# Optimization experiments

Measured on AMD Instinct MI355X. Metric: run time of the kernel, lower is better.

Reference implementation:

```python
import jax, jax.numpy as jnp
import numpy as np

IN, E, BSZ, A, J, NC, BATCH = 784, 512, 8, 2, 7, 128, 512
T = BSZ ** A  # 64 blocks


def setup_inputs() -> dict:
    key = jax.random.key(0)
    ks = jax.random.split(key, 10)
    s = lambda k, sh: (jax.random.normal(k, sh, jnp.float32) * 0.02)
    return {
        "x": jax.random.normal(ks[0], (BATCH, IN), jnp.float32),
        "emb_W": s(ks[1], (IN, E)), "emb_b": jnp.zeros((E,), jnp.float32),
        # stacked per-block state_transform: Linear(E,E)-ReLU-Linear(E,E)-ReLU
        "st_W1": s(ks[2], (T, E, E)), "st_b1": jnp.zeros((T, E), jnp.float32),
        "st_W2": s(ks[3], (T, E, E)), "st_b2": jnp.zeros((T, E), jnp.float32),
        # stacked per-block address_transform: Linear(E,E)-ReLU-Linear(E,A*BSZ)
        "ad_W1": s(ks[4], (T, E, E)), "ad_b1": jnp.zeros((T, E), jnp.float32),
        "ad_W2": s(ks[5], (T, E, A * BSZ)), "ad_b2": jnp.zeros((T, A * BSZ), jnp.float32),
        # output head: Linear(E,E)-ReLU-Linear(E,NC)
        "out_W1": s(ks[6], (E, E)), "out_b1": jnp.zeros((E,), jnp.float32),
        "out_W2": s(ks[7], (E, NC)), "out_b2": jnp.zeros((NC,), jnp.float32),
    }


def reference(x, emb_W, emb_b, st_W1, st_b1, st_W2, st_b2,
              ad_W1, ad_b1, ad_W2, ad_b2, out_W1, out_b1, out_W2, out_b2):
    strides = BSZ ** jnp.arange(A - 1, -1, -1)  # row-major flat index

    def flat_idx(addr):  # [B, A] -> [B]
        return jnp.sum(addr * strides, axis=1)

    def next_address(state, idx):
        # block's address_transform; argmax(softmax(logits)) == argmax(logits)
        h = jax.nn.relu(jnp.einsum("be,beh->bh", state, ad_W1[idx]) + ad_b1[idx])
        logits = jnp.einsum("bh,bho->bo", h, ad_W2[idx]) + ad_b2[idx]
        return jnp.argmax(logits.reshape(-1, A, BSZ), axis=2)  # [B, A]

    def through_block(state, idx):
        h = jax.nn.relu(jnp.einsum("be,beh->bh", state, st_W1[idx]) + st_b1[idx])
        t = jax.nn.relu(jnp.einsum("bh,bho->bo", h, st_W2[idx]) + st_b2[idx])
        norm = jnp.linalg.norm(state, axis=1, keepdims=True)
        return t / (norm + 1e-6)

    state = x.reshape(x.shape[0], -1) @ emb_W + emb_b  # [B, E]
    initial_state = state
    B = state.shape[0]
    # initial address from brain_blocks[0]
    addr = next_address(initial_state, jnp.zeros((B,), jnp.int32))

    for i in range(J):  # small fixed jump count
        idx = flat_idx(addr)
        t = through_block(state, idx)           # normalized transformed state
        addr = next_address(t, idx)             # address from transformed state
        state = t + (i / max(1, J - 1)) * initial_state  # residual ramp

    final = through_block(state, flat_idx(addr)) + initial_state
    h = jax.nn.relu(final @ out_W1 + out_b1)
    return h @ out_W2 + out_b2  # [B, NC]
```

## Files before the change

kernel.cpp:

```cpp
#include <hip/hip_runtime.h>

namespace {

constexpr int B     = 512;
constexpr int IN_F  = 784;
constexpr int E     = 512;
constexpr int ABSZ  = 16;
constexpr int J     = 7;
constexpr int NC    = 128;
constexpr int NT    = 256;

__device__ inline void matvec512(const float* __restrict__ W,
                                 const float* __restrict__ bias,
                                 const float* __restrict__ vin,
                                 float* __restrict__ vout,
                                 int tid, bool do_relu)
{
    const int o = 2 * tid;
    float a0 = 0.f, a1 = 0.f;
    const float* wp = W + o;
    #pragma unroll 8
    for (int e = 0; e < E; ++e) {
        const float v = vin[e];
        const float2 w = *reinterpret_cast<const float2*>(wp + (size_t)e * E);
        a0 = fmaf(v, w.x, a0);
        a1 = fmaf(v, w.y, a1);
    }
    a0 += bias[o];
    a1 += bias[o + 1];
    if (do_relu) { a0 = fmaxf(a0, 0.f); a1 = fmaxf(a1, 0.f); }
    vout[o]     = a0;
    vout[o + 1] = a1;
}

__device__ inline int next_address(const float* __restrict__ ad_W1,
                                   const float* __restrict__ ad_b1,
                                   const float* __restrict__ ad_W2,
                                   const float* __restrict__ ad_b2,
                                   int idx,
                                   const float* __restrict__ vin,
                                   float* __restrict__ s_h,
                                   float* __restrict__ s_part,
                                   float* __restrict__ s_logits,
                                   int* __restrict__ s_idx_p,
                                   int tid)
{
    matvec512(ad_W1 + (size_t)idx * E * E, ad_b1 + (size_t)idx * E, vin, s_h, tid, true);
    __syncthreads();

    {
        const int o  = tid & (ABSZ - 1);
        const int e0 = tid >> 4;
        const float* w2 = ad_W2 + (size_t)idx * E * ABSZ;
        float acc = 0.f;
        #pragma unroll 4
        for (int e = e0; e < E; e += 16) {
            acc = fmaf(s_h[e], w2[(size_t)e * ABSZ + o], acc);
        }
        s_part[tid] = acc;
    }
    __syncthreads();
    if (tid < ABSZ) {
        float sum = ad_b2[(size_t)idx * ABSZ + tid];
        #pragma unroll
        for (int k = 0; k < 16; ++k) sum += s_part[tid + 16 * k];
        s_logits[tid] = sum;
    }
    __syncthreads();
    if (tid == 0) {
        int a0 = 0, a1 = 0;
        float m0 = s_logits[0], m1 = s_logits[8];
        #pragma unroll
        for (int k = 1; k < 8; ++k) {
            if (s_logits[k]     > m0) { m0 = s_logits[k];     a0 = k; }
            if (s_logits[8 + k] > m1) { m1 = s_logits[8 + k]; a1 = k; }
        }
        *s_idx_p = a0 * 8 + a1;
    }
    __syncthreads();
    return *s_idx_p;
}

__device__ inline void through_block(const float* __restrict__ st_W1,
                                     const float* __restrict__ st_b1,
                                     const float* __restrict__ st_W2,
                                     const float* __restrict__ st_b2,
                                     int idx,
                                     const float* __restrict__ s_state,
                                     float* __restrict__ s_h,
                                     float* __restrict__ s_t,
                                     float* __restrict__ s_part,
                                     float* __restrict__ s_scale,
                                     int tid)
{
    matvec512(st_W1 + (size_t)idx * E * E, st_b1 + (size_t)idx * E, s_state, s_h, tid, true);

    {
        const int o = 2 * tid;
        float v0 = s_state[o], v1 = s_state[o + 1];
        float ss = v0 * v0 + v1 * v1;
        #pragma unroll
        for (int off = 32; off > 0; off >>= 1) ss += __shfl_down(ss, off, 64);
        if ((tid & 63) == 0) s_part[tid >> 6] = ss;
    }
    __syncthreads();
    if (tid == 0) {
        float tot = s_part[0] + s_part[1] + s_part[2] + s_part[3];
        *s_scale = 1.0f / (sqrtf(tot) + 1e-6f);
    }
    matvec512(st_W2 + (size_t)idx * E * E, st_b2 + (size_t)idx * E, s_h, s_t, tid, true);
    __syncthreads();
    {
        const float sc = *s_scale;
        const int o = 2 * tid;
        s_t[o]     *= sc;
        s_t[o + 1] *= sc;
    }
    __syncthreads();
}

__global__ __launch_bounds__(NT) void brain_kernel(
    const float* __restrict__ x,
    const float* __restrict__ emb_W,  const float* __restrict__ emb_b,
    const float* __restrict__ st_W1,  const float* __restrict__ st_b1,
    const float* __restrict__ st_W2,  const float* __restrict__ st_b2,
    const float* __restrict__ ad_W1,  const float* __restrict__ ad_b1,
    const float* __restrict__ ad_W2,  const float* __restrict__ ad_b2,
    const float* __restrict__ out_W1, const float* __restrict__ out_b1,
    const float* __restrict__ out_W2, const float* __restrict__ out_b2,
    float* __restrict__ out)
{
    const int b   = blockIdx.x;
    const int tid = threadIdx.x;

    __shared__ float s_x[IN_F];
    __shared__ float s_state[E];
    __shared__ float s_init[E];
    __shared__ float s_h[E];
    __shared__ float s_t[E];
    __shared__ float s_part[NT];
    __shared__ float s_logits[ABSZ];
    __shared__ float s_scale;
    __shared__ int   s_idx;

    for (int i = tid; i < IN_F; i += NT) s_x[i] = x[(size_t)b * IN_F + i];
    __syncthreads();

    {
        const int o = 2 * tid;
        float a0 = 0.f, a1 = 0.f;
        const float* wp = emb_W + o;
        #pragma unroll 4
        for (int i = 0; i < IN_F; ++i) {
            const float v = s_x[i];
            const float2 w = *reinterpret_cast<const float2*>(wp + (size_t)i * E);
            a0 = fmaf(v, w.x, a0);
            a1 = fmaf(v, w.y, a1);
        }
        a0 += emb_b[o];
        a1 += emb_b[o + 1];
        s_state[o]     = a0;  s_state[o + 1] = a1;
        s_init[o]      = a0;  s_init[o + 1]  = a1;
    }
    __syncthreads();

    int idx = next_address(ad_W1, ad_b1, ad_W2, ad_b2, 0, s_init,
                           s_h, s_part, s_logits, &s_idx, tid);

    for (int i = 0; i < J; ++i) {
        through_block(st_W1, st_b1, st_W2, st_b2, idx,
                      s_state, s_h, s_t, s_part, &s_scale, tid);
        const int nidx = next_address(ad_W1, ad_b1, ad_W2, ad_b2, idx, s_t,
                                      s_h, s_part, s_logits, &s_idx, tid);
        {
            const float ramp = (float)i * (1.0f / 6.0f);
            const int o = 2 * tid;
            s_state[o]     = s_t[o]     + ramp * s_init[o];
            s_state[o + 1] = s_t[o + 1] + ramp * s_init[o + 1];
        }
        __syncthreads();
        idx = nidx;
    }

    through_block(st_W1, st_b1, st_W2, st_b2, idx,
                  s_state, s_h, s_t, s_part, &s_scale, tid);
    {
        const int o = 2 * tid;
        s_state[o]     = s_t[o]     + s_init[o];
        s_state[o + 1] = s_t[o + 1] + s_init[o + 1];
    }
    __syncthreads();

    matvec512(out_W1, out_b1, s_state, s_h, tid, true);
    __syncthreads();

    {
        const int oo = tid & (NC - 1);
        const int e0 = tid >> 7;
        float acc = 0.f;
        #pragma unroll 4
        for (int e = e0; e < E; e += 2) {
            acc = fmaf(s_h[e], out_W2[(size_t)e * NC + oo], acc);
        }
        s_part[tid] = acc;
    }
    __syncthreads();
    if (tid < NC) {
        out[(size_t)b * NC + tid] = out_b2[tid] + s_part[tid] + s_part[tid + NC];
    }
}

}

extern "C" void kernel_launch(void* const* d_in, const int* in_sizes, int n_in,
                              void* d_out, int out_size, void* d_ws, size_t ws_size,
                              hipStream_t stream)
{
    const float* x      = (const float*)d_in[0];
    const float* emb_W  = (const float*)d_in[1];
    const float* emb_b  = (const float*)d_in[2];
    const float* st_W1  = (const float*)d_in[3];
    const float* st_b1  = (const float*)d_in[4];
    const float* st_W2  = (const float*)d_in[5];
    const float* st_b2  = (const float*)d_in[6];
    const float* ad_W1  = (const float*)d_in[7];
    const float* ad_b1  = (const float*)d_in[8];
    const float* ad_W2  = (const float*)d_in[9];
    const float* ad_b2  = (const float*)d_in[10];
    const float* out_W1 = (const float*)d_in[11];
    const float* out_b1 = (const float*)d_in[12];
    const float* out_W2 = (const float*)d_in[13];
    const float* out_b2 = (const float*)d_in[14];
    float* out = (float*)d_out;

    hipLaunchKernelGGL(brain_kernel, dim3(B), dim3(NT), 0, stream,
                       x, emb_W, emb_b, st_W1, st_b1, st_W2, st_b2,
                       ad_W1, ad_b1, ad_W2, ad_b2,
                       out_W1, out_b1, out_W2, out_b2, out);
}
```

Measured before the change: 1.755 ms.

## Replace per-sample fused kernel with bucketed multi-kernel batched matvec pipeline

The single per-sample kernel, which streamed a full 512x512 weight matrix per sample per layer, is replaced by a sequence of kernels. Each jump now groups samples by their block index (bucket kernel), so every weight tile is loaded once and applied to up to eight rows of the same block. Norm, residual ramp and argmax are folded into small per-row kernels. This cuts weight traffic roughly by the bucket occupancy, at the cost of about 40 kernel launches, a single-block bucketing step with a serial prefix scan, and intermediates round-tripping through global memory.

```diff
diff --git a/kernel.cpp b/kernel.cpp
--- a/kernel.cpp
+++ b/kernel.cpp
@@ -2,72 +2,197 @@
 
 namespace {
 
-constexpr int B     = 512;
-constexpr int IN_F  = 784;
-constexpr int E     = 512;
-constexpr int ABSZ  = 16;
-constexpr int J     = 7;
-constexpr int NC    = 128;
-constexpr int NT    = 256;
-
-__device__ inline void matvec512(const float* __restrict__ W,
-                                 const float* __restrict__ bias,
-                                 const float* __restrict__ vin,
-                                 float* __restrict__ vout,
-                                 int tid, bool do_relu)
-{
-    const int o = 2 * tid;
-    float a0 = 0.f, a1 = 0.f;
-    const float* wp = W + o;
-    #pragma unroll 8
-    for (int e = 0; e < E; ++e) {
-        const float v = vin[e];
-        const float2 w = *reinterpret_cast<const float2*>(wp + (size_t)e * E);
-        a0 = fmaf(v, w.x, a0);
-        a1 = fmaf(v, w.y, a1);
-    }
-    a0 += bias[o];
-    a1 += bias[o + 1];
-    if (do_relu) { a0 = fmaxf(a0, 0.f); a1 = fmaxf(a1, 0.f); }
-    vout[o]     = a0;
-    vout[o + 1] = a1;
-}
-
-__device__ inline int next_address(const float* __restrict__ ad_W1,
-                                   const float* __restrict__ ad_b1,
-                                   const float* __restrict__ ad_W2,
-                                   const float* __restrict__ ad_b2,
-                                   int idx,
-                                   const float* __restrict__ vin,
-                                   float* __restrict__ s_h,
-                                   float* __restrict__ s_part,
-                                   float* __restrict__ s_logits,
-                                   int* __restrict__ s_idx_p,
-                                   int tid)
-{
-    matvec512(ad_W1 + (size_t)idx * E * E, ad_b1 + (size_t)idx * E, vin, s_h, tid, true);
+constexpr int B      = 512;
+constexpr int IN_F   = 784;
+constexpr int E      = 512;
+constexpr int T      = 64;
+constexpr int ABSZ   = 16;
+constexpr int J      = 7;
+constexpr int NC     = 128;
+constexpr int TILE_R = 8;
+constexpr int MAXTIL = 128;
+
+__global__ void k_iddesc(int* __restrict__ rows_id, int4* __restrict__ desc_id)
+{
+    const int t = threadIdx.x;
+    rows_id[t] = t;
+    if (t < MAXTIL)
+        desc_id[t] = (t < B / TILE_R) ? make_int4(0, t * TILE_R, TILE_R, 0)
+                                      : make_int4(0, 0, 0, 0);
+}
+
+__global__ __launch_bounds__(256) void k_embed(
+    const float* __restrict__ x, const float* __restrict__ Wm,
+    const float* __restrict__ bias,
+    float* __restrict__ state, float* __restrict__ initv)
+{
+    const int c  = blockIdx.y * 256 + threadIdx.x;
+    const int r0 = blockIdx.x * 8;
+    float acc[8] = {0,0,0,0,0,0,0,0};
+    const float* Wb = Wm + c;
+    for (int e = 0; e < IN_F; e += 4) {
+        const float w0 = Wb[(size_t)(e + 0) * E];
+        const float w1 = Wb[(size_t)(e + 1) * E];
+        const float w2 = Wb[(size_t)(e + 2) * E];
+        const float w3 = Wb[(size_t)(e + 3) * E];
+        #pragma unroll
+        for (int g = 0; g < 8; ++g) {
+            const float4 xv = *reinterpret_cast<const float4*>(
+                x + (size_t)(r0 + g) * IN_F + e);
+            acc[g] = fmaf(xv.x, w0, acc[g]);
+            acc[g] = fmaf(xv.y, w1, acc[g]);
+            acc[g] = fmaf(xv.z, w2, acc[g]);
+            acc[g] = fmaf(xv.w, w3, acc[g]);
+        }
+    }
+    const float bv = bias[c];
+    #pragma unroll
+    for (int g = 0; g < 8; ++g) {
+        const float v = acc[g] + bv;
+        state[(size_t)(r0 + g) * E + c] = v;
+        initv[(size_t)(r0 + g) * E + c] = v;
+    }
+}
+
+__global__ __launch_bounds__(64) void k_norm(const float* __restrict__ state,
+                                             float* __restrict__ norms)
+{
+    const int row = blockIdx.x;
+    const int t   = threadIdx.x;
+    const float4 a = *reinterpret_cast<const float4*>(state + (size_t)row * E + t * 8);
+    const float4 b = *reinterpret_cast<const float4*>(state + (size_t)row * E + t * 8 + 4);
+    float ss = a.x*a.x + a.y*a.y + a.z*a.z + a.w*a.w
+             + b.x*b.x + b.y*b.y + b.z*b.z + b.w*b.w;
+    #pragma unroll
+    for (int off = 32; off > 0; off >>= 1) ss += __shfl_down(ss, off, 64);
+    if (t == 0) norms[row] = sqrtf(ss);
+}
+
+__global__ __launch_bounds__(512) void k_bucket(const int* __restrict__ idx,
+                                                int* __restrict__ rows_sorted,
+                                                int4* __restrict__ desc)
+{
+    __shared__ int cnt[T], off[T], c2[T];
+    const int t = threadIdx.x;
+    if (t < T) { cnt[t] = 0; c2[t] = 0; }
     __syncthreads();
-
-    {
-        const int o  = tid & (ABSZ - 1);
-        const int e0 = tid >> 4;
-        const float* w2 = ad_W2 + (size_t)idx * E * ABSZ;
-        float acc = 0.f;
-        #pragma unroll 4
-        for (int e = e0; e < E; e += 16) {
-            acc = fmaf(s_h[e], w2[(size_t)e * ABSZ + o], acc);
-        }
-        s_part[tid] = acc;
-    }
+    const int my = idx[t];
+    atomicAdd(&cnt[my], 1);
     __syncthreads();
-    if (tid < ABSZ) {
-        float sum = ad_b2[(size_t)idx * ABSZ + tid];
-        #pragma unroll
-        for (int k = 0; k < 16; ++k) sum += s_part[tid + 16 * k];
-        s_logits[tid] = sum;
+    if (t == 0) {
+        int s = 0;
+        for (int b = 0; b < T; ++b) { off[b] = s; s += cnt[b]; }
     }
     __syncthreads();
-    if (tid == 0) {
+    const int p = off[my] + atomicAdd(&c2[my], 1);
+    rows_sorted[p] = t;
+    if (t == 0) {
+        int slot = 0;
+        for (int b = 0; b < T; ++b) {
+            const int G = cnt[b], o = off[b];
+            for (int k = 0; k < G; k += TILE_R)
+                desc[slot++] = make_int4(b, o + k, min(TILE_R, G - k), 0);
+        }
+        for (; slot < MAXTIL; ++slot) desc[slot] = make_int4(0, 0, 0, 0);
+    }
+}
+
+template <bool RELU, bool SCALE, bool ADDINIT>
+__global__ __launch_bounds__(256) void k_mv(
+    const float* __restrict__ in, float* __restrict__ out,
+    const float* __restrict__ W, const float* __restrict__ bias,
+    const int4* __restrict__ desc, const int* __restrict__ rows,
+    const float* __restrict__ norms, const float* __restrict__ initv)
+{
+    const int4 d = desc[blockIdx.x];
+    const int n = d.z;
+    if (n == 0) return;
+    const int blk = d.x, start = d.y;
+    const int c = blockIdx.y * 256 + threadIdx.x;
+    const float* Wb = W + (size_t)blk * E * E + c;
+
+    int rowid[TILE_R];
+    int rbase[TILE_R];
+    #pragma unroll
+    for (int g = 0; g < TILE_R; ++g) {
+        rowid[g] = rows[start + min(g, n - 1)];
+        rbase[g] = rowid[g] * E;
+    }
+
+    float acc[TILE_R] = {0,0,0,0,0,0,0,0};
+    for (int e = 0; e < E; e += 4) {
+        const float w0 = Wb[(size_t)(e + 0) * E];
+        const float w1 = Wb[(size_t)(e + 1) * E];
+        const float w2 = Wb[(size_t)(e + 2) * E];
+        const float w3 = Wb[(size_t)(e + 3) * E];
+        #pragma unroll
+        for (int g = 0; g < TILE_R; ++g) {
+            const float4 sv = *reinterpret_cast<const float4*>(in + rbase[g] + e);
+            acc[g] = fmaf(sv.x, w0, acc[g]);
+            acc[g] = fmaf(sv.y, w1, acc[g]);
+            acc[g] = fmaf(sv.z, w2, acc[g]);
+            acc[g] = fmaf(sv.w, w3, acc[g]);
+        }
+    }
+
+    const float bv = bias[blk * E + c];
+    #pragma unroll
+    for (int g = 0; g < TILE_R; ++g) {
+        if (g < n) {
+            float v = acc[g] + bv;
+            if (RELU) v = fmaxf(v, 0.f);
+            if (SCALE) v *= 1.0f / (norms[rowid[g]] + 1e-6f);
+            if (ADDINIT) v += initv[(size_t)rbase[g] + c];
+            out[(size_t)rbase[g] + c] = v;
+        }
+    }
+}
+
+template <bool UPDATE, bool FIXED0>
+__global__ __launch_bounds__(64) void k_small(
+    const float* __restrict__ gin, const float* __restrict__ W2,
+    const float* __restrict__ b2, int* __restrict__ idx,
+    const float* __restrict__ tin, const float* __restrict__ initv,
+    float* __restrict__ state, float* __restrict__ norms, float ramp)
+{
+    const int row = blockIdx.x;
+    const int t   = threadIdx.x;
+    const int blk = FIXED0 ? 0 : idx[row];
+    const int o   = t & 15;
+    const int p   = t >> 4;
+
+    float acc = 0.f;
+    const float* w2 = W2 + (size_t)blk * E * ABSZ;
+    const float* gr = gin + (size_t)row * E;
+    for (int e = p; e < E; e += 4)
+        acc = fmaf(gr[e], w2[(size_t)e * ABSZ + o], acc);
+    acc += __shfl_down(acc, 32, 64);
+    acc += __shfl_down(acc, 16, 64);
+
+    __shared__ float s_logits[ABSZ];
+    if (t < ABSZ) s_logits[t] = acc + b2[(size_t)blk * ABSZ + t];
+
+    float ss = 0.f;
+    if (UPDATE) {
+        const float4 tv0 = *reinterpret_cast<const float4*>(tin  + (size_t)row * E + t * 8);
+        const float4 tv1 = *reinterpret_cast<const float4*>(tin  + (size_t)row * E + t * 8 + 4);
+        const float4 iv0 = *reinterpret_cast<const float4*>(initv + (size_t)row * E + t * 8);
+        const float4 iv1 = *reinterpret_cast<const float4*>(initv + (size_t)row * E + t * 8 + 4);
+        float4 n0, n1;
+        n0.x = tv0.x + ramp * iv0.x;  n0.y = tv0.y + ramp * iv0.y;
+        n0.z = tv0.z + ramp * iv0.z;  n0.w = tv0.w + ramp * iv0.w;
+        n1.x = tv1.x + ramp * iv1.x;  n1.y = tv1.y + ramp * iv1.y;
+        n1.z = tv1.z + ramp * iv1.z;  n1.w = tv1.w + ramp * iv1.w;
+        *reinterpret_cast<float4*>(state + (size_t)row * E + t * 8)     = n0;
+        *reinterpret_cast<float4*>(state + (size_t)row * E + t * 8 + 4) = n1;
+        ss = n0.x*n0.x + n0.y*n0.y + n0.z*n0.z + n0.w*n0.w
+           + n1.x*n1.x + n1.y*n1.y + n1.z*n1.z + n1.w*n1.w;
+        #pragma unroll
+        for (int off2 = 32; off2 > 0; off2 >>= 1) ss += __shfl_down(ss, off2, 64);
+    }
+
+    __syncthreads();
+    if (t == 0) {
         int a0 = 0, a1 = 0;
         float m0 = s_logits[0], m1 = s_logits[8];
         #pragma unroll
@@ -75,139 +200,37 @@
             if (s_logits[k]     > m0) { m0 = s_logits[k];     a0 = k; }
             if (s_logits[8 + k] > m1) { m1 = s_logits[8 + k]; a1 = k; }
         }
-        *s_idx_p = a0 * 8 + a1;
-    }
-    __syncthreads();
-    return *s_idx_p;
-}
-
-__device__ inline void through_block(const float* __restrict__ st_W1,
-                                     const float* __restrict__ st_b1,
-                                     const float* __restrict__ st_W2,
-                                     const float* __restrict__ st_b2,
-                                     int idx,
-                                     const float* __restrict__ s_state,
-                                     float* __restrict__ s_h,
-                                     float* __restrict__ s_t,
-                                     float* __restrict__ s_part,
-                                     float* __restrict__ s_scale,
-                                     int tid)
-{
-    matvec512(st_W1 + (size_t)idx * E * E, st_b1 + (size_t)idx * E, s_state, s_h, tid, true);
-
-    {
-        const int o = 2 * tid;
-        float v0 = s_state[o], v1 = s_state[o + 1];
-        float ss = v0 * v0 + v1 * v1;
-        #pragma unroll
-        for (int off = 32; off > 0; off >>= 1) ss += __shfl_down(ss, off, 64);
-        if ((tid & 63) == 0) s_part[tid >> 6] = ss;
-    }
-    __syncthreads();
-    if (tid == 0) {
-        float tot = s_part[0] + s_part[1] + s_part[2] + s_part[3];
-        *s_scale = 1.0f / (sqrtf(tot) + 1e-6f);
-    }
-    matvec512(st_W2 + (size_t)idx * E * E, st_b2 + (size_t)idx * E, s_h, s_t, tid, true);
-    __syncthreads();
-    {
-        const float sc = *s_scale;
-        const int o = 2 * tid;
-        s_t[o]     *= sc;
-        s_t[o + 1] *= sc;
-    }
-    __syncthreads();
-}
-
-__global__ __launch_bounds__(NT) void brain_kernel(
-    const float* __restrict__ x,
-    const float* __restrict__ emb_W,  const float* __restrict__ emb_b,
-    const float* __restrict__ st_W1,  const float* __restrict__ st_b1,
-    const float* __restrict__ st_W2,  const float* __restrict__ st_b2,
-    const float* __restrict__ ad_W1,  const float* __restrict__ ad_b1,
-    const float* __restrict__ ad_W2,  const float* __restrict__ ad_b2,
-    const float* __restrict__ out_W1, const float* __restrict__ out_b1,
-    const float* __restrict__ out_W2, const float* __restrict__ out_b2,
-    float* __restrict__ out)
-{
-    const int b   = blockIdx.x;
-    const int tid = threadIdx.x;
-
-    __shared__ float s_x[IN_F];
-    __shared__ float s_state[E];
-    __shared__ float s_init[E];
-    __shared__ float s_h[E];
-    __shared__ float s_t[E];
-    __shared__ float s_part[NT];
-    __shared__ float s_logits[ABSZ];
-    __shared__ float s_scale;
-    __shared__ int   s_idx;
-
-    for (int i = tid; i < IN_F; i += NT) s_x[i] = x[(size_t)b * IN_F + i];
-    __syncthreads();
-
-    {
-        const int o = 2 * tid;
-        float a0 = 0.f, a1 = 0.f;
-        const float* wp = emb_W + o;
-        #pragma unroll 4
-        for (int i = 0; i < IN_F; ++i) {
-            const float v = s_x[i];
-            const float2 w = *reinterpret_cast<const float2*>(wp + (size_t)i * E);
-            a0 = fmaf(v, w.x, a0);
-            a1 = fmaf(v, w.y, a1);
-        }
-        a0 += emb_b[o];
-        a1 += emb_b[o + 1];
-        s_state[o]     = a0;  s_state[o + 1] = a1;
-        s_init[o]      = a0;  s_init[o + 1]  = a1;
-    }
-    __syncthreads();
-
-    int idx = next_address(ad_W1, ad_b1, ad_W2, ad_b2, 0, s_init,
-                           s_h, s_part, s_logits, &s_idx, tid);
-
-    for (int i = 0; i < J; ++i) {
-        through_block(st_W1, st_b1, st_W2, st_b2, idx,
-                      s_state, s_h, s_t, s_part, &s_scale, tid);
-        const int nidx = next_address(ad_W1, ad_b1, ad_W2, ad_b2, idx, s_t,
-                                      s_h, s_part, s_logits, &s_idx, tid);
-        {
-            const float ramp = (float)i * (1.0f / 6.0f);
-            const int o = 2 * tid;
-            s_state[o]     = s_t[o]     + ramp * s_init[o];
-            s_state[o + 1] = s_t[o + 1] + ramp * s_init[o + 1];
-        }
-        __syncthreads();
-        idx = nidx;
-    }
-
-    through_block(st_W1, st_b1, st_W2, st_b2, idx,
-                  s_state, s_h, s_t, s_part, &s_scale, tid);
-    {
-        const int o = 2 * tid;
-        s_state[o]     = s_t[o]     + s_init[o];
-        s_state[o + 1] = s_t[o + 1] + s_init[o + 1];
-    }
-    __syncthreads();
-
-    matvec512(out_W1, out_b1, s_state, s_h, tid, true);
-    __syncthreads();
-
-    {
-        const int oo = tid & (NC - 1);
-        const int e0 = tid >> 7;
-        float acc = 0.f;
-        #pragma unroll 4
-        for (int e = e0; e < E; e += 2) {
-            acc = fmaf(s_h[e], out_W2[(size_t)e * NC + oo], acc);
-        }
-        s_part[tid] = acc;
-    }
-    __syncthreads();
-    if (tid < NC) {
-        out[(size_t)b * NC + tid] = out_b2[tid] + s_part[tid] + s_part[tid + NC];
-    }
+        idx[row] = a0 * 8 + a1;
+        if (UPDATE) norms[row] = sqrtf(ss);
+    }
+}
+
+__global__ __launch_bounds__(128) void k_out(
+    const float* __restrict__ h, const float* __restrict__ W,
+    const float* __restrict__ bias, float* __restrict__ out)
+{
+    const int c  = threadIdx.x;
+    const int r0 = blockIdx.x * 8;
+    float acc[8] = {0,0,0,0,0,0,0,0};
+    for (int e = 0; e < E; e += 4) {
+        const float w0 = W[(size_t)(e + 0) * NC + c];
+        const float w1 = W[(size_t)(e + 1) * NC + c];
+        const float w2 = W[(size_t)(e + 2) * NC + c];
+        const float w3 = W[(size_t)(e + 3) * NC + c];
+        #pragma unroll
+        for (int g = 0; g < 8; ++g) {
+            const float4 hv = *reinterpret_cast<const float4*>(
+                h + (size_t)(r0 + g) * E + e);
+            acc[g] = fmaf(hv.x, w0, acc[g]);
+            acc[g] = fmaf(hv.y, w1, acc[g]);
+            acc[g] = fmaf(hv.z, w2, acc[g]);
+            acc[g] = fmaf(hv.w, w3, acc[g]);
+        }
+    }
+    const float bv = bias[c];
+    #pragma unroll
+    for (int g = 0; g < 8; ++g)
+        out[(size_t)(r0 + g) * NC + c] = acc[g] + bv;
 }
 
 }
@@ -233,8 +256,52 @@
     const float* out_b2 = (const float*)d_in[14];
     float* out = (float*)d_out;
 
-    hipLaunchKernelGGL(brain_kernel, dim3(B), dim3(NT), 0, stream,
-                       x, emb_W, emb_b, st_W1, st_b1, st_W2, st_b2,
-                       ad_W1, ad_b1, ad_W2, ad_b2,
-                       out_W1, out_b1, out_W2, out_b2, out);
-}
+    float* ws    = (float*)d_ws;
+    float* state = ws;
+    float* initv = ws + 1 * 262144;
+    float* tbuf  = ws + 2 * 262144;
+    float* hbuf  = ws + 3 * 262144;
+    float* norms = ws + 4 * 262144;
+    int*   idx         = (int*)(norms + 512);
+    int*   rows_sorted = idx + 512;
+    int4*  desc        = (int4*)(rows_sorted + 512);
+    int*   rows_id     = (int*)(desc + MAXTIL);
+    int4*  desc_id     = (int4*)(rows_id + 512);
+
+    const dim3 mv_grid(MAXTIL, 2);
+
+    hipLaunchKernelGGL(k_iddesc, dim3(1), dim3(512), 0, stream, rows_id, desc_id);
+    hipLaunchKernelGGL(k_embed, dim3(64, 2), dim3(256), 0, stream,
+                       x, emb_W, emb_b, state, initv);
+    hipLaunchKernelGGL(k_norm, dim3(B), dim3(64), 0, stream, state, norms);
+
+    hipLaunchKernelGGL((k_mv<true, false, false>), mv_grid, dim3(256), 0, stream,
+                       state, hbuf, ad_W1, ad_b1, desc_id, rows_id, norms, initv);
+    hipLaunchKernelGGL((k_small<false, true>), dim3(B), dim3(64), 0, stream,
+                       hbuf, ad_W2, ad_b2, idx, tbuf, initv, state, norms, 0.f);
+
+    for (int i = 0; i < J; ++i) {
+        const float ramp = (float)i * (1.0f / 6.0f);
+        hipLaunchKernelGGL(k_bucket, dim3(1), dim3(512), 0, stream,
+                           idx, rows_sorted, desc);
+        hipLaunchKernelGGL((k_mv<true, false, false>), mv_grid, dim3(256), 0, stream,
+                           state, hbuf, st_W1, st_b1, desc, rows_sorted, norms, initv);
+        hipLaunchKernelGGL((k_mv<true, true, false>), mv_grid, dim3(256), 0, stream,
+                           hbuf, tbuf, st_W2, st_b2, desc, rows_sorted, norms, initv);
+        hipLaunchKernelGGL((k_mv<true, false, false>), mv_grid, dim3(256), 0, stream,
+                           tbuf, hbuf, ad_W1, ad_b1, desc, rows_sorted, norms, initv);
+        hipLaunchKernelGGL((k_small<true, false>), dim3(B), dim3(64), 0, stream,
+                           hbuf, ad_W2, ad_b2, idx, tbuf, initv, state, norms, ramp);
+    }
+
+    hipLaunchKernelGGL(k_bucket, dim3(1), dim3(512), 0, stream,
+                       idx, rows_sorted, desc);
+    hipLaunchKernelGGL((k_mv<true, false, false>), mv_grid, dim3(256), 0, stream,
+                       state, hbuf, st_W1, st_b1, desc, rows_sorted, norms, initv);
+    hipLaunchKernelGGL((k_mv<true, true, true>), mv_grid, dim3(256), 0, stream,
+                       hbuf, state, st_W2, st_b2, desc, rows_sorted, norms, initv);
+    hipLaunchKernelGGL((k_mv<true, false, false>), mv_grid, dim3(256), 0, stream,
+                       state, hbuf, out_W1, out_b1, desc_id, rows_id, norms, initv);
+    hipLaunchKernelGGL(k_out, dim3(64), dim3(128), 0, stream,
+                       hbuf, out_W2, out_b2, out);
+}
```

Result: slower. 2.196 ms (+25.1%).
